# Kernel optimization log

Measured on AMD Instinct MI355X. Metric: run time of the kernel, lower is better.

## Reference

```python
import jax, jax.numpy as jnp
import numpy as np

THRESH = 1.0
EPS = 1e-5  # nn.LayerNorm default eps
T, H, C, K = 16384, 1024, 256, 3


def setup_inputs() -> dict:
    key = jax.random.key(0)
    ks = jax.random.split(key, 4)
    encoder_out = jax.random.normal(ks[0], (1, T, H), jnp.float32)
    conv_w = jax.random.normal(ks[1], (C, H, K), jnp.float32) * (1.0 / np.sqrt(H * K))
    conv_b = jnp.zeros((C,), jnp.float32)
    ln_g = jnp.ones((C,), jnp.float32)
    ln_b = jnp.zeros((C,), jnp.float32)
    lin_w = jax.random.normal(ks[2], (1, C), jnp.float32) * (1.0 / np.sqrt(C))
    lin_b = jnp.zeros((1,), jnp.float32)
    return dict(encoder_out=encoder_out, conv_w=conv_w, conv_b=conv_b,
                ln_g=ln_g, ln_b=ln_b, lin_w=lin_w, lin_b=lin_b)


def _cif(encoder_out, conv_w, conv_b, ln_g, ln_b, lin_w, lin_b):
    # encoder_out: [1, T, H]  (torch code only supports B=1 due to tensor bool())
    x = jnp.transpose(encoder_out, (0, 2, 1))                     # [1, H, T]
    conv = jax.lax.conv_general_dilated(
        x, conv_w, window_strides=(1,), padding=[(1, 1)],
        dimension_numbers=('NCH', 'OIH', 'NCH')) + conv_b[None, :, None]
    conv = jnp.transpose(conv, (0, 2, 1))                         # [1, T, C]
    mu = conv.mean(-1, keepdims=True)
    var = conv.var(-1, keepdims=True)
    ln = (conv - mu) / jnp.sqrt(var + EPS) * ln_g + ln_b
    h = jax.nn.relu(ln)
    alpha = jax.nn.sigmoid(h @ lin_w.T + lin_b)                   # [1, T, 1]
    alphas = alpha.sum(axis=1)[:, None, :]                        # [1, 1, 1] (torch stacks one sum)

    a = alpha[0, :, 0]                                            # [T]
    xs = encoder_out[0]                                           # [T, H]

    def step(carry, inp):
        acc_a, acc_f = carry
        at, xt = inp
        s = acc_a + at
        fire = s >= THRESH
        a_u1 = 1.0 - acc_a            # == 1 - (s - at)
        fired_feat = acc_f + a_u1 * xt
        a_u2 = at - a_u1
        new_a = jnp.where(fire, a_u2, s)
        new_f = jnp.where(fire, a_u2 * xt, acc_f + at * xt)
        return (new_a, new_f), (fire, jnp.where(fire, fired_feat, jnp.zeros_like(fired_feat)))

    init = (jnp.float32(0.0), jnp.zeros((H,), encoder_out.dtype))
    (fin_a, fin_f), (fires, feats) = jax.lax.scan(step, init, (a, xs))

    # compact fired features into a [T+1, H] padded buffer (data-independent shape)
    cnt = jnp.cumsum(fires.astype(jnp.int32))                     # [T]
    idx = jnp.where(fires, cnt - 1, T)                            # dump non-fires into pad slot
    out = jnp.zeros((T + 1, H), encoder_out.dtype).at[idx].add(feats)
    n_fires = cnt[-1]
    # trailing residual: appended iff current_alpha_sum > 0
    out = out.at[n_fires].add(jnp.where(fin_a > 0.0, fin_f, jnp.zeros_like(fin_f)))
    return out[None], alphas                                      # [1, T+1, H], [1, 1, 1]


def reference(encoder_out, conv_w, conv_b, ln_g, ln_b, lin_w, lin_b):
    return _cif(encoder_out, conv_w, conv_b, ln_g, ln_b, lin_w, lin_b)
```

## Files before the change

### kernel.cpp

```cpp
#include <hip/hip_runtime.h>
#include <math.h>

#define T_LEN 16384
#define H_DIM 1024
#define C_DIM 256
#define BKC 16


__global__ __launch_bounds__(256) void kwt(const float* __restrict__ w,
                                           float* __restrict__ wt) {
  int idx = blockIdx.x * 256 + threadIdx.x;
  int h = idx >> 8;
  int c = idx & 255;
  const float* s = w + ((size_t)c * H_DIM + h) * 3;
  float a0 = s[0], a1 = s[1], a2 = s[2];
  wt[((size_t)0 * H_DIM + h) * C_DIM + c] = a0;
  wt[((size_t)1 * H_DIM + h) * C_DIM + c] = a1;
  wt[((size_t)2 * H_DIM + h) * C_DIM + c] = a2;
}

__global__ __launch_bounds__(256) void kconv(
    const float* __restrict__ x, const float* __restrict__ wt,
    float* __restrict__ part)
{
  __shared__ float As[BKC][68];
  __shared__ float Bs[3][BKC][128];
  const int tid  = threadIdx.x;
  const int tile = blockIdx.x >> 1;
  const int ch   = blockIdx.x & 1;
  const int t0   = tile * 64;
  const int c0   = ch * 128;
  const int i = tid >> 5;
  const int j = tid & 31;
  const int wv   = tid >> 6;
  const int lane = tid & 63;

  float acc[8][4];
  #pragma unroll
  for (int a0 = 0; a0 < 8; ++a0)
    #pragma unroll
    for (int b0 = 0; b0 < 4; ++b0) acc[a0][b0] = 0.f;

  const int tloc = tid >> 2;
  const int hg   = tid & 3;

  for (int kt = 0; kt < 64; ++kt) {
    const int h0 = kt * BKC;

    float4 areg0 = make_float4(0.f, 0.f, 0.f, 0.f), areg1 = areg0;
    {
      const int tr = t0 + tloc - 1;
      if (tr >= 0 && tr < T_LEN)
        areg0 = *(const float4*)(x + (size_t)tr * H_DIM + h0 + 4 * hg);
      if (tid < 8) {
        const int tl2 = 64 + (tid >> 2);
        const int tr2 = t0 + tl2 - 1;
        if (tr2 >= 0 && tr2 < T_LEN)
          areg1 = *(const float4*)(x + (size_t)tr2 * H_DIM + h0 + 4 * (tid & 3));
      }
    }
    __syncthreads();

    #pragma unroll
    for (int it = 0; it < 6; ++it) {
      const int r  = 6 * wv + it;
      const int dl = r >> 3;
      const int kk = (r & 7) * 2;
      const float* src = wt + ((size_t)dl * H_DIM + h0 + kk + (lane >> 5)) * C_DIM
                            + c0 + 4 * (lane & 31);
      __builtin_amdgcn_global_load_lds(
          (const __attribute__((address_space(1))) unsigned int*)src,
          (__attribute__((address_space(3))) unsigned int*)&Bs[dl][kk][0],
          16, 0, 0);
    }
    As[4 * hg + 0][tloc] = areg0.x; As[4 * hg + 1][tloc] = areg0.y;
    As[4 * hg + 2][tloc] = areg0.z; As[4 * hg + 3][tloc] = areg0.w;
    if (tid < 8) {
      const int tl2 = 64 + (tid >> 2), hg2 = (tid & 3) * 4;
      As[hg2 + 0][tl2] = areg1.x; As[hg2 + 1][tl2] = areg1.y;
      As[hg2 + 2][tl2] = areg1.z; As[hg2 + 3][tl2] = areg1.w;
    }
    __syncthreads();

    #pragma unroll
    for (int k = 0; k < BKC; ++k) {
      float aw[10];
      *(float4*)&aw[0] = *(const float4*)&As[k][8 * i];
      *(float4*)&aw[4] = *(const float4*)&As[k][8 * i + 4];
      *(float2*)&aw[8] = *(const float2*)&As[k][8 * i + 8];
      float bw[3][4];
      #pragma unroll
      for (int dl = 0; dl < 3; ++dl)
        *(float4*)&bw[dl][0] = *(const float4*)&Bs[dl][k][4 * j];
      #pragma unroll
      for (int ii = 0; ii < 8; ++ii)
        #pragma unroll
        for (int qq = 0; qq < 4; ++qq)
          acc[ii][qq] = fmaf(aw[ii],     bw[0][qq],
                        fmaf(aw[ii + 1], bw[1][qq],
                        fmaf(aw[ii + 2], bw[2][qq], acc[ii][qq])));
    }
  }

  #pragma unroll
  for (int ii = 0; ii < 8; ++ii) {
    const size_t t = t0 + 8 * i + ii;
    *(float4*)&part[t * C_DIM + c0 + 4 * j] =
        make_float4(acc[ii][0], acc[ii][1], acc[ii][2], acc[ii][3]);
  }
}

__global__ __launch_bounds__(64) void kadd(
    const float* __restrict__ part, const float* __restrict__ cb,
    const float* __restrict__ lng, const float* __restrict__ lnb,
    const float* __restrict__ lw, const float* __restrict__ lb,
    float* __restrict__ alpha)
{
  const int row = blockIdx.x;
  const int l = threadIdx.x;
  const float4 p0 = *(const float4*)&part[(size_t)row * C_DIM + 4 * l];
  const float4 cb4 = *(const float4*)&cb[4 * l];
  float v[4] = {p0.x + cb4.x, p0.y + cb4.y, p0.z + cb4.z, p0.w + cb4.w};
  float s = v[0] + v[1] + v[2] + v[3];
  #pragma unroll
  for (int m = 1; m < 64; m <<= 1) s += __shfl_xor(s, m, 64);
  const float mu = s * (1.0f / 256.0f);
  float ss = 0.f;
  #pragma unroll
  for (int q = 0; q < 4; ++q) { const float d = v[q] - mu; ss += d * d; }
  #pragma unroll
  for (int m = 1; m < 64; m <<= 1) ss += __shfl_xor(ss, m, 64);
  const float rstd = 1.0f / sqrtf(ss * (1.0f / 256.0f) + 1e-5f);
  const float4 g4 = *(const float4*)&lng[4 * l];
  const float4 b4 = *(const float4*)&lnb[4 * l];
  const float4 w4 = *(const float4*)&lw[4 * l];
  const float gg[4] = {g4.x, g4.y, g4.z, g4.w};
  const float bb[4] = {b4.x, b4.y, b4.z, b4.w};
  const float ww[4] = {w4.x, w4.y, w4.z, w4.w};
  float dot = 0.f;
  #pragma unroll
  for (int q = 0; q < 4; ++q) {
    float h = (v[q] - mu) * rstd * gg[q] + bb[q];
    h = fmaxf(h, 0.f);
    dot = fmaf(h, ww[q], dot);
  }
  #pragma unroll
  for (int m = 1; m < 64; m <<= 1) dot += __shfl_xor(dot, m, 64);
  if (l == 0)
    alpha[row] = 1.0f / (1.0f + expf(-(dot + lb[0])));
}

__global__ __launch_bounds__(256) void kscan(const float* __restrict__ alpha,
                                             float* __restrict__ atr)
{
  __shared__ float sa[T_LEN + 64];
  const int tid = threadIdx.x;
  #pragma unroll
  for (int b = 0; b < 16; ++b)
    ((float4*)sa)[b * 256 + tid] = ((const float4*)alpha)[b * 256 + tid];
  if (tid < 16)
    ((float4*)sa)[4096 + tid] = make_float4(0.f, 0.f, 0.f, 0.f);
  __syncthreads();
  if (tid != 0) return;

  const float4* sa4 = (const float4*)sa;
  float acc = 0.f;
  float4 A[8], B[8];
  #pragma unroll
  for (int b = 0; b < 8; ++b) A[b] = sa4[b];

#define CIF_STEP(at, dst)                              \
  {                                                    \
    const float s_   = acc + (at);                     \
    const float au1_ = 1.0f - acc;                     \
    const float au2_ = (at) - au1_;                    \
    acc = (s_ >= 1.0f) ? au2_ : s_;                    \
    (dst) = acc;                                       \
  }

  for (int t = 0; t < T_LEN; t += 64) {
    const int q = t >> 2;
    #pragma unroll
    for (int b = 0; b < 8; ++b) B[b] = sa4[q + 8 + b];
    #pragma unroll
    for (int b = 0; b < 8; ++b) {
      const float4 v = A[b];
      float4 o;
      CIF_STEP(v.x, o.x); CIF_STEP(v.y, o.y);
      CIF_STEP(v.z, o.z); CIF_STEP(v.w, o.w);
      *(float4*)&atr[t + 4 * b] = o;
    }
    #pragma unroll
    for (int b = 0; b < 8; ++b) A[b] = sa4[q + 16 + b];
    #pragma unroll
    for (int b = 0; b < 8; ++b) {
      const float4 v = B[b];
      float4 o;
      CIF_STEP(v.x, o.x); CIF_STEP(v.y, o.y);
      CIF_STEP(v.z, o.z); CIF_STEP(v.w, o.w);
      *(float4*)&atr[t + 32 + 4 * b] = o;
    }
  }
#undef CIF_STEP
}

__global__ __launch_bounds__(256) void kscan2(
    const float* __restrict__ alpha, const float* __restrict__ atr,
    int* __restrict__ fire_t, float* __restrict__ wu1, float* __restrict__ wu2,
    int* __restrict__ meta, float* __restrict__ alphas_out)
{
  __shared__ int wsum[4];
  __shared__ float fsum[4];
  const int tid = threadIdx.x;
  const int lane = tid & 63, wv = tid >> 6;
  const unsigned long long bl = (1ull << lane) - 1ull;
  int gbase = 0;
  float asum = 0.f;
  for (int it = 0; it < 16; ++it) {
    const int tb = it * 1024 + tid * 4;
    const float4 a4 = *(const float4*)&alpha[tb];
    const float4 t4 = *(const float4*)&atr[tb];
    const float prev0 = (tb == 0) ? 0.f : atr[tb - 1];
    const float pv[4] = {prev0, t4.x, t4.y, t4.z};
    const float av[4] = {a4.x, a4.y, a4.z, a4.w};
    bool f[4];
    #pragma unroll
    for (int u = 0; u < 4; ++u) {
      f[u] = (pv[u] + av[u] >= 1.0f);
      asum += av[u];
    }
    unsigned long long m[4];
    #pragma unroll
    for (int u = 0; u < 4; ++u) m[u] = __ballot(f[u]);
    if (lane == 0)
      wsum[wv] = __popcll(m[0]) + __popcll(m[1]) + __popcll(m[2]) + __popcll(m[3]);
    __syncthreads();
    int wbase = gbase, total = 0;
    #pragma unroll
    for (int w = 0; w < 4; ++w) {
      if (w < wv) wbase += wsum[w];
      total += wsum[w];
    }
    const int lanepre = __popcll(m[0] & bl) + __popcll(m[1] & bl) +
                        __popcll(m[2] & bl) + __popcll(m[3] & bl);
    int sub = 0;
    #pragma unroll
    for (int u = 0; u < 4; ++u) {
      if (f[u]) {
        const int idx = wbase + lanepre + sub;
        fire_t[idx] = tb + u;
        const float au1 = 1.0f - pv[u];
        wu1[idx] = au1;
        wu2[idx] = av[u] - au1;
        ++sub;
      }
    }
    gbase += total;
    __syncthreads();
  }
  #pragma unroll
  for (int m2 = 1; m2 < 64; m2 <<= 1) asum += __shfl_xor(asum, m2, 64);
  if (lane == 0) fsum[wv] = asum;
  __syncthreads();
  if (tid == 0) {
    alphas_out[0] = fsum[0] + fsum[1] + fsum[2] + fsum[3];
    meta[0] = gbase;
    meta[1] = (atr[T_LEN - 1] > 0.0f) ? 1 : 0;
  }
}

__global__ __launch_bounds__(256) void kscat(
    const float* __restrict__ x, const float* __restrict__ alpha,
    const int* __restrict__ fire_t, const float* __restrict__ wu1,
    const float* __restrict__ wu2, const int* __restrict__ meta,
    float* __restrict__ out)
{
  const int r = blockIdx.x;
  const int tid = threadIdx.x;
  const int nf = meta[0];
  float4 acc = make_float4(0.f, 0.f, 0.f, 0.f);
  if (r < nf || (r == nf && meta[1])) {
    const bool isfin = (r == nf);
    const int tprev = (r > 0) ? fire_t[r - 1] : -1;
    const int tend = isfin ? (T_LEN - 1) : fire_t[r];
    const float wprev = (r > 0) ? wu2[r - 1] : 0.f;
    const float wlast = isfin ? 0.f : wu1[r];
    for (int t = (tprev < 0 ? 0 : tprev); t <= tend; ++t) {
      float w;
      if (!isfin && t == tend)      w = wlast;
      else if (t == tprev)          w = wprev;
      else                          w = alpha[t];
      const float4 xv = ((const float4*)x)[(size_t)t * 256 + tid];
      acc.x = fmaf(w, xv.x, acc.x);
      acc.y = fmaf(w, xv.y, acc.y);
      acc.z = fmaf(w, xv.z, acc.z);
      acc.w = fmaf(w, xv.w, acc.w);
    }
  }
  ((float4*)out)[(size_t)r * 256 + tid] = acc;
}

extern "C" void kernel_launch(void* const* d_in, const int* in_sizes, int n_in,
                              void* d_out, int out_size, void* d_ws, size_t ws_size,
                              hipStream_t stream) {
  const float* enc   = (const float*)d_in[0];
  const float* convw = (const float*)d_in[1];
  const float* convb = (const float*)d_in[2];
  const float* lng   = (const float*)d_in[3];
  const float* lnb   = (const float*)d_in[4];
  const float* linw  = (const float*)d_in[5];
  const float* linb  = (const float*)d_in[6];
  float* out = (float*)d_out;

  float* ws     = (float*)d_ws;
  float* wt     = ws;
  float* alpha  = ws + 786432;
  int*   fire_t = (int*)(ws + 802816);
  float* wu1    = ws + 819200;
  float* wu2    = ws + 835584;
  int*   meta   = (int*)(ws + 851968);
  float* atr    = ws + 851976;

  float* part = out;

  hipLaunchKernelGGL(kwt,    dim3(1024),  dim3(256), 0, stream, convw, wt);
  hipLaunchKernelGGL(kconv,  dim3(512),   dim3(256), 0, stream, enc, wt, part);
  hipLaunchKernelGGL(kadd,   dim3(16384), dim3(64),  0, stream,
                     part, convb, lng, lnb, linw, linb, alpha);
  hipLaunchKernelGGL(kscan,  dim3(1),     dim3(256), 0, stream, alpha, atr);
  hipLaunchKernelGGL(kscan2, dim3(1),     dim3(256), 0, stream,
                     alpha, atr, fire_t, wu1, wu2, meta, out + (size_t)16385 * 1024);
  hipLaunchKernelGGL(kscat,  dim3(16385), dim3(256), 0, stream,
                     enc, alpha, fire_t, wu1, wu2, meta, out);
}
```

Baseline: 720.3 us.

## Double-buffer conv GEMM shared tiles to overlap global loads with compute

Doubles the A and B shared-memory tiles in the conv kernel so the next K-slice is loaded while the current one is computed. This cuts one of the two barriers per iteration. The prefetched A registers are written to LDS midway through the compute to hide global latency. The cost is twice the LDS footprint, which may lower occupancy, plus the extra live prefetch registers.

```diff
diff --git a/kernel.cpp b/kernel.cpp
--- a/kernel.cpp
+++ b/kernel.cpp
@@ -23,8 +23,8 @@
     const float* __restrict__ x, const float* __restrict__ wt,
     float* __restrict__ part)
 {
-  __shared__ float As[BKC][68];
-  __shared__ float Bs[3][BKC][128];
+  __shared__ float As[2][BKC][68];
+  __shared__ float Bs[2][3][BKC][128];
   const int tid  = threadIdx.x;
   const int tile = blockIdx.x >> 1;
   const int ch   = blockIdx.x & 1;
@@ -43,62 +43,81 @@
 
   const int tloc = tid >> 2;
   const int hg   = tid & 3;
-
-  for (int kt = 0; kt < 64; ++kt) {
-    const int h0 = kt * BKC;
-
-    float4 areg0 = make_float4(0.f, 0.f, 0.f, 0.f), areg1 = areg0;
+  const int tr   = t0 + tloc - 1;
+  const bool trok = (tr >= 0 && tr < T_LEN);
+  const int tl2  = 64 + (tid >> 2);
+  const int tr2  = t0 + tl2 - 1;
+  const bool tr2ok = (tid < 8) && (tr2 < T_LEN);
+
+  float4 areg0, areg1;
+
+#define A_LOAD(H0)                                                            \
+  areg0 = make_float4(0.f, 0.f, 0.f, 0.f); areg1 = areg0;                     \
+  if (trok)  areg0 = *(const float4*)(x + (size_t)tr  * H_DIM + (H0) + 4*hg); \
+  if (tr2ok) areg1 = *(const float4*)(x + (size_t)tr2 * H_DIM + (H0) + 4*(tid&3));
+
+#define A_WRITE(BUF)                                                          \
+  As[BUF][4*hg+0][tloc] = areg0.x; As[BUF][4*hg+1][tloc] = areg0.y;           \
+  As[BUF][4*hg+2][tloc] = areg0.z; As[BUF][4*hg+3][tloc] = areg0.w;           \
+  if (tid < 8) {                                                              \
+    const int hg2 = (tid & 3) * 4;                                            \
+    As[BUF][hg2+0][tl2] = areg1.x; As[BUF][hg2+1][tl2] = areg1.y;             \
+    As[BUF][hg2+2][tl2] = areg1.z; As[BUF][hg2+3][tl2] = areg1.w;             \
+  }
+
+#define B_ISSUE(H0, BUF)                                                      \
+  _Pragma("unroll")                                                           \
+  for (int it = 0; it < 6; ++it) {                                            \
+    const int r  = 6 * wv + it;                                    \
+    const int dl = r >> 3;                                      \
+    const int kk = (r & 7) * 2;                        \
+    const float* src = wt + ((size_t)dl * H_DIM + (H0) + kk + (lane >> 5)) * C_DIM \
+                          + c0 + 4 * (lane & 31);                             \
+    __builtin_amdgcn_global_load_lds(                                         \
+        (const __attribute__((address_space(1))) unsigned int*)src,           \
+        (__attribute__((address_space(3))) unsigned int*)&Bs[BUF][dl][kk][0], \
+        16, 0, 0);                                                            \
+  }
+
+#define COMPUTE8(BUF, KLO)                                                    \
+  _Pragma("unroll")                                                           \
+  for (int k = (KLO); k < (KLO) + 8; ++k) {                                   \
+    float aw[10];                                                             \
+    *(float4*)&aw[0] = *(const float4*)&As[BUF][k][8 * i];                    \
+    *(float4*)&aw[4] = *(const float4*)&As[BUF][k][8 * i + 4];                \
+    *(float2*)&aw[8] = *(const float2*)&As[BUF][k][8 * i + 8];                \
+    float bw[3][4];                                                           \
+    _Pragma("unroll")                                                         \
+    for (int dl = 0; dl < 3; ++dl)                                            \
+      *(float4*)&bw[dl][0] = *(const float4*)&Bs[BUF][dl][k][4 * j];          \
+    _Pragma("unroll")                                                         \
+    for (int ii = 0; ii < 8; ++ii)                                            \
+      _Pragma("unroll")                                                       \
+      for (int qq = 0; qq < 4; ++qq)                                          \
+        acc[ii][qq] = fmaf(aw[ii],     bw[0][qq],                             \
+                      fmaf(aw[ii + 1], bw[1][qq],                             \
+                      fmaf(aw[ii + 2], bw[2][qq], acc[ii][qq])));             \
+  }
+
+  A_LOAD(0); B_ISSUE(0, 0); A_WRITE(0);
+  __syncthreads();
+
+  for (int kt = 0; kt < 64; kt += 2) {
     {
-      const int tr = t0 + tloc - 1;
-      if (tr >= 0 && tr < T_LEN)
-        areg0 = *(const float4*)(x + (size_t)tr * H_DIM + h0 + 4 * hg);
-      if (tid < 8) {
-        const int tl2 = 64 + (tid >> 2);
-        const int tr2 = t0 + tl2 - 1;
-        if (tr2 >= 0 && tr2 < T_LEN)
-          areg1 = *(const float4*)(x + (size_t)tr2 * H_DIM + h0 + 4 * (tid & 3));
-      }
-    }
-    __syncthreads();
-
-    #pragma unroll
-    for (int it = 0; it < 6; ++it) {
-      const int r  = 6 * wv + it;
-      const int dl = r >> 3;
-      const int kk = (r & 7) * 2;
-      const float* src = wt + ((size_t)dl * H_DIM + h0 + kk + (lane >> 5)) * C_DIM
-                            + c0 + 4 * (lane & 31);
-      __builtin_amdgcn_global_load_lds(
-          (const __attribute__((address_space(1))) unsigned int*)src,
-          (__attribute__((address_space(3))) unsigned int*)&Bs[dl][kk][0],
-          16, 0, 0);
-    }
-    As[4 * hg + 0][tloc] = areg0.x; As[4 * hg + 1][tloc] = areg0.y;
-    As[4 * hg + 2][tloc] = areg0.z; As[4 * hg + 3][tloc] = areg0.w;
-    if (tid < 8) {
-      const int tl2 = 64 + (tid >> 2), hg2 = (tid & 3) * 4;
-      As[hg2 + 0][tl2] = areg1.x; As[hg2 + 1][tl2] = areg1.y;
-      As[hg2 + 2][tl2] = areg1.z; As[hg2 + 3][tl2] = areg1.w;
-    }
-    __syncthreads();
-
-    #pragma unroll
-    for (int k = 0; k < BKC; ++k) {
-      float aw[10];
-      *(float4*)&aw[0] = *(const float4*)&As[k][8 * i];
-      *(float4*)&aw[4] = *(const float4*)&As[k][8 * i + 4];
-      *(float2*)&aw[8] = *(const float2*)&As[k][8 * i + 8];
-      float bw[3][4];
-      #pragma unroll
-      for (int dl = 0; dl < 3; ++dl)
-        *(float4*)&bw[dl][0] = *(const float4*)&Bs[dl][k][4 * j];
-      #pragma unroll
-      for (int ii = 0; ii < 8; ++ii)
-        #pragma unroll
-        for (int qq = 0; qq < 4; ++qq)
-          acc[ii][qq] = fmaf(aw[ii],     bw[0][qq],
-                        fmaf(aw[ii + 1], bw[1][qq],
-                        fmaf(aw[ii + 2], bw[2][qq], acc[ii][qq])));
+      const int h1 = (kt + 1) * BKC;
+      A_LOAD(h1); B_ISSUE(h1, 1);
+      COMPUTE8(0, 0);
+      A_WRITE(1);
+      COMPUTE8(0, 8);
+      __syncthreads();
+    }
+    {
+      const int h2 = (kt + 2) * BKC;
+      if (kt + 2 < 64) { A_LOAD(h2); B_ISSUE(h2, 0); }
+      COMPUTE8(1, 0);
+      if (kt + 2 < 64) { A_WRITE(0); }
+      COMPUTE8(1, 8);
+      __syncthreads();
     }
   }
 
@@ -108,6 +127,10 @@
     *(float4*)&part[t * C_DIM + c0 + 4 * j] =
         make_float4(acc[ii][0], acc[ii][1], acc[ii][2], acc[ii][3]);
   }
+#undef A_LOAD
+#undef A_WRITE
+#undef B_ISSUE
+#undef COMPUTE8
 }
 
 __global__ __launch_bounds__(64) void kadd(
```

Measured after the change: 812.2 us. 1.13x slower.
